# Kernel optimization log

Hardware: AMD Instinct MI355X
Metric: run time of the kernel (lower is better)

Reference implementation:

```python
import jax, jax.numpy as jnp
import numpy as np
import math

NUM_HEADS = 4
PH, PW = 8, 8

def setup_inputs() -> dict:
    key = jax.random.key(0)
    ks = jax.random.split(key, 12)
    B, C, H, W = 2, 128, 256, 256
    x = jax.random.normal(ks[0], (B, C, H, W), dtype=jnp.float32)
    mask = jax.random.uniform(ks[1], (B, 1, H, W), dtype=jnp.float32)
    s1 = 1.0 / math.sqrt(C)          # kaiming-ish scale for 1x1 convs
    s3 = 1.0 / math.sqrt(C * 9)      # 3x3 conv
    wq = jax.random.normal(ks[2], (C, C), dtype=jnp.float32) * s1
    bq = jax.random.normal(ks[3], (C,), dtype=jnp.float32) * 0.01
    wk = jax.random.normal(ks[4], (C, C), dtype=jnp.float32) * s1
    bk = jax.random.normal(ks[5], (C,), dtype=jnp.float32) * 0.01
    wv = jax.random.normal(ks[6], (C, C), dtype=jnp.float32) * s1
    bv = jax.random.normal(ks[7], (C,), dtype=jnp.float32) * 0.01
    wo = jax.random.normal(ks[8], (C, C, 3, 3), dtype=jnp.float32) * s3
    bo = jax.random.normal(ks[9], (C,), dtype=jnp.float32) * 0.01
    return {"x": x, "mask": mask, "wq": wq, "bq": bq, "wk": wk, "bk": bk,
            "wv": wv, "bv": bv, "wo": wo, "bo": bo}

def _conv1x1(x, w, b):
    # w: [O, I]; x: [B, C, H, W]
    return jnp.einsum('oc,bchw->bohw', w, x) + b[None, :, None, None]

def _window(t, b, heads, dph, out_h, out_w):
    # [B, C, H, W] -> [B, heads, out_h*out_w, dph*PH*PW]
    t = t.reshape(b, heads, dph, out_h, PH, out_w, PW)
    t = t.transpose(0, 1, 3, 5, 2, 4, 6)
    return t.reshape(b, heads, out_h * out_w, dph * PH * PW)

def reference(x, mask, wq, bq, wk, bk, wv, bv, wo, bo):
    b, c, h, w = x.shape
    heads = NUM_HEADS
    dph = c // heads
    out_h, out_w = h // PH, w // PW
    d = dph * PH * PW

    q = _window(_conv1x1(x, wq, bq), b, heads, dph, out_h, out_w)
    k = _window(_conv1x1(x, wk, bk), b, heads, dph, out_h, out_w)
    v = _window(_conv1x1(x, wv, bv), b, heads, dph, out_h, out_w)

    # NOTE: original torch code calls att.masked_fill(mask, -1e9) without
    # assignment (not in-place), so the mask has no effect on the output.
    att = jnp.einsum('bhqd,bhkd->bhqk', q, k) * (1.0 / math.sqrt(d))
    p = jax.nn.softmax(att, axis=-1)
    y = jnp.einsum('bhqk,bhkd->bhqd', p, v)

    # un-window: [B, heads, S, d] -> [B, C, H, W]
    y = y.reshape(b, heads, out_h, out_w, dph, PH, PW)
    y = y.transpose(0, 1, 4, 2, 5, 3, 6).reshape(b, c, h, w)

    # output: reflect-padded 3x3 conv + LeakyReLU(0.2)
    yp = jnp.pad(y, ((0, 0), (0, 0), (1, 1), (1, 1)), mode='reflect')
    out = jax.lax.conv_general_dilated(
        yp, wo, window_strides=(1, 1), padding='VALID',
        dimension_numbers=('NCHW', 'OIHW', 'NCHW')) + bo[None, :, None, None]
    return jnp.where(out > 0, out, 0.2 * out)
```

## Files before the change

kernel.cpp:

```cpp
#include <hip/hip_runtime.h>
#include <hip/hip_bf16.h>
#include <stdint.h>

typedef unsigned short u16;
typedef __attribute__((ext_vector_type(8))) short bf16x8;
typedef __attribute__((ext_vector_type(4))) short bf16x4;
typedef __attribute__((ext_vector_type(4))) float f32x4;
typedef __attribute__((ext_vector_type(4))) unsigned short u16x4;

__device__ __forceinline__ float bf2f(u16 u) {
  union { unsigned i; float f; } c; c.i = ((unsigned)u) << 16; return c.f;
}
__device__ __forceinline__ u16 f2bf(float f) {
  union { float f; unsigned i; } c; c.f = f;
  unsigned r = c.i + 0x7FFFu + ((c.i >> 16) & 1u);
  return (u16)(r >> 16);
}
__device__ __forceinline__ unsigned cvt_pk(float lo, float hi) {
  unsigned r;
  asm("v_cvt_pk_bf16_f32 %0, %1, %2" : "=v"(r) : "v"(lo), "v"(hi));
  return r;
}
__device__ __forceinline__ void gl2lds16(const u16* g, u16* l) {
  __builtin_amdgcn_global_load_lds(
      (const __attribute__((address_space(1))) unsigned int*)(uintptr_t)g,
      (__attribute__((address_space(3))) unsigned int*)(uintptr_t)l,
      16, 0, 0);
}

__global__ void k_prep(const float* __restrict__ wo, const float* __restrict__ wq,
                       const float* __restrict__ wk, const float* __restrict__ wv,
                       u16* __restrict__ WT, u16* __restrict__ WQKV) {
  int i = blockIdx.x * 256 + threadIdx.x;
  if (i < 9 * 128 * 128) {
    int c = i & 127;
    int o = (i >> 7) & 127;
    int tap = i >> 14;
    WT[i] = f2bf(wo[((o * 128 + c) * 3 + tap / 3) * 3 + tap % 3]);
  } else {
    int j = i - 9 * 128 * 128;
    if (j < 3 * 16384) {
      int sel = j >> 14, rest = j & 16383;
      const float* w = sel == 0 ? wq : (sel == 1 ? wk : wv);
      WQKV[j] = f2bf(w[rest]);
    }
  }
}

__global__ __launch_bounds__(256) void k_qkv(
    const float* __restrict__ x, const u16* __restrict__ WQKV,
    const float* __restrict__ bq, const float* __restrict__ bk,
    const float* __restrict__ bv,
    u16* __restrict__ Q, u16* __restrict__ K, u16* __restrict__ V) {
  const int blk = blockIdx.x;
  const int b = blk >> 9;
  const int t = blk & 511;
  const int th = t & 31, tw = t >> 5;
  const int h0 = th * 8, w0 = tw * 16;
  const int s0 = th * 32 + tw * 2;
  const int tid = threadIdx.x, lane = tid & 63, wid = tid >> 6;
  const int wr = wid >> 1, wc = wid & 1;
  const int g = lane >> 4, l15 = lane & 15;

  __shared__ u16 Ot[128 * 136];

  bf16x8 bfrag[4][4];
  {
    const float* xb = x + (size_t)b * 8388608 + (size_t)(g * 8) * 65536
                        + (h0 + wc * 4) * 256 + w0 + l15;
    #pragma unroll
    for (int ks = 0; ks < 4; ++ks)
      #pragma unroll
      for (int e2 = 0; e2 < 4; ++e2) {
        const float* pa = xb + (size_t)(ks * 32 + e2 * 2) * 65536;
        const float* pb = pa + 65536;
        #pragma unroll
        for (int n = 0; n < 4; ++n)
          ((unsigned*)&bfrag[ks][n])[e2] = cvt_pk(pa[n * 256], pb[n * 256]);
      }
  }

  for (int sel = 0; sel < 3; ++sel) {
    const u16* w = WQKV + sel * 16384;
    const float* bias = sel == 0 ? bq : (sel == 1 ? bk : bv);
    u16* qkv = sel == 0 ? Q : (sel == 1 ? K : V);

    f32x4 acc[4][4] = {};
    #pragma unroll
    for (int ks = 0; ks < 4; ++ks) {
      bf16x8 a[4];
      #pragma unroll
      for (int m = 0; m < 4; ++m) {
        int o = wr * 64 + m * 16 + l15;
        a[m] = *(const bf16x8*)(w + o * 128 + ks * 32 + g * 8);
      }
      #pragma unroll
      for (int m = 0; m < 4; ++m)
        #pragma unroll
        for (int n = 0; n < 4; ++n)
          acc[m][n] = __builtin_amdgcn_mfma_f32_16x16x32_bf16(a[m], bfrag[ks][n], acc[m][n], 0, 0, 0);
    }

    float4 bias4[4];
    #pragma unroll
    for (int m = 0; m < 4; ++m)
      bias4[m] = *(const float4*)&bias[wr * 64 + m * 16 + g * 4];

    __syncthreads();
    #pragma unroll
    for (int m = 0; m < 4; ++m) {
      int o0 = wr * 64 + m * 16 + g * 4;
      #pragma unroll
      for (int n = 0; n < 4; ++n) {
        int p = wc * 64 + n * 16 + l15;
        unsigned r0 = cvt_pk(acc[m][n][0] + bias4[m].x, acc[m][n][1] + bias4[m].y);
        unsigned r1 = cvt_pk(acc[m][n][2] + bias4[m].z, acc[m][n][3] + bias4[m].w);
        unsigned* dp = (unsigned*)&Ot[p * 136 + o0];
        dp[0] = r0; dp[1] = r1;
      }
    }
    __syncthreads();
    #pragma unroll
    for (int it = 0; it < 8; ++it) {
      int head = it >> 1, s2 = it & 1;
      int pixw = tid >> 2;
      int dphc = tid & 3;
      int pl = (pixw >> 3) * 16 + s2 * 8 + (pixw & 7);
      bf16x8 vv = *(const bf16x8*)&Ot[pl * 136 + head * 32 + dphc * 8];
      size_t gaddr = ((size_t)((b * 4 + head) * 1024 + s0 + s2)) * 2048 + pixw * 32 + dphc * 8;
      *(bf16x8*)(qkv + gaddr) = vv;
    }
  }
}

__global__ __launch_bounds__(256) void k_qkvt(const u16* __restrict__ Q,
                                              const u16* __restrict__ K,
                                              u16* __restrict__ ATT,
                                              const u16* __restrict__ V,
                                              u16* __restrict__ VT) {
  __shared__ __align__(16) u16 smem[17408];
  const int tid = threadIdx.x, lane = tid & 63, wid = tid >> 6;

  if (blockIdx.x < 512) {
    const int bh = blockIdx.x & 7;
    const int tile = blockIdx.x >> 3;
    const int tm = tile & 7, tn = tile >> 3;
    const int row0 = tm * 128, col0 = tn * 128;
    const int wr = wid >> 1, wc = wid & 1;
    const u16* Ab = Q + (size_t)bh * 1024 * 2048 + (size_t)row0 * 2048;
    const u16* Bb = K + (size_t)bh * 1024 * 2048 + (size_t)col0 * 2048;
    f32x4 acc[4][4] = {};
    const int lr = lane >> 2, lc = lane & 3;
    const int scs = lc ^ ((lr >> 1) & 3);
    const int rsw = ((lane & 15) >> 1) & 3;

    auto stage = [&](int k0, int bf) {
      u16* As = smem + bf * 8192;
      u16* Bs = smem + 4096 + bf * 8192;
      const u16* s0 = Ab + (size_t)(wid * 16 + lr) * 2048 + k0 + scs * 8;
      gl2lds16(s0, &As[wid * 512]);
      gl2lds16(s0 + (size_t)64 * 2048, &As[2048 + wid * 512]);
      const u16* s1 = Bb + (size_t)(wid * 16 + lr) * 2048 + k0 + scs * 8;
      gl2lds16(s1, &Bs[wid * 512]);
      gl2lds16(s1 + (size_t)64 * 2048, &Bs[2048 + wid * 512]);
    };

    stage(0, 0);
    asm volatile("s_waitcnt vmcnt(0)" ::: "memory");
    __syncthreads();
    int cur = 0;
    for (int k0 = 0; k0 < 2048; k0 += 32) {
      if (k0 + 32 < 2048) stage(k0 + 32, cur ^ 1);
      const u16* As = smem + cur * 8192;
      const u16* Bs = smem + 4096 + cur * 8192;
      bf16x8 a[4], bb[4];
      const int g = lane >> 4;
      const int chp = (g ^ rsw) * 8;
      #pragma unroll
      for (int m = 0; m < 4; ++m)
        a[m] = *(const bf16x8*)&As[(wr * 64 + m * 16 + (lane & 15)) * 32 + chp];
      #pragma unroll
      for (int n = 0; n < 4; ++n)
        bb[n] = *(const bf16x8*)&Bs[(wc * 64 + n * 16 + (lane & 15)) * 32 + chp];
      #pragma unroll
      for (int m = 0; m < 4; ++m)
        #pragma unroll
        for (int n = 0; n < 4; ++n)
          acc[m][n] = __builtin_amdgcn_mfma_f32_16x16x32_bf16(a[m], bb[n], acc[m][n], 0, 0, 0);
      asm volatile("s_waitcnt vmcnt(0)" ::: "memory");
      __syncthreads();
      cur ^= 1;
    }
    const float scale = 0.02209708691207961f;
    u16* Ot = smem;
    #pragma unroll
    for (int m = 0; m < 4; ++m) {
      int r0 = wr * 64 + m * 16 + ((lane >> 4) << 2);
      #pragma unroll
      for (int n = 0; n < 4; ++n) {
        int dv = wc * 64 + n * 16 + (lane & 15);
        #pragma unroll
        for (int j = 0; j < 4; ++j)
          Ot[(r0 + j) * 136 + dv] = f2bf(acc[m][n][j] * scale);
      }
    }
    __syncthreads();
    u16* outb = ATT + (size_t)bh * 1024 * 1024 + (size_t)row0 * 1024 + col0;
    #pragma unroll
    for (int it = 0; it < 8; ++it) {
      int ci = it * 256 + tid;
      int sl = ci >> 4;
      int ch = ci & 15;
      bf16x8 vv = *(const bf16x8*)&Ot[sl * 136 + ch * 8];
      *(bf16x8*)(outb + (size_t)sl * 1024 + ch * 8) = vv;
    }
  } else {
    const int idx = blockIdx.x - 512;
    const int bh = idx & 7;
    const int t2 = idx >> 3;
    const int ts = t2 & 7, td = t2 >> 3;
    const int s0 = ts * 128, d0 = td * 128;
    u16* T = smem;
    const u16* Vb = V + (size_t)bh * 1024 * 2048 + (size_t)s0 * 2048 + d0;

    #pragma unroll
    for (int pass = 0; pass < 8; ++pass) {
      int r = pass * 16 + (tid >> 4);
      int c8 = (tid & 15) * 8;
      union { uint4 u; u16 e[8]; } d;
      d.u = *(const uint4*)(Vb + (size_t)r * 2048 + c8);
      int chunk = (r >> 3) ^ ((c8 >> 3) & 15);
      #pragma unroll
      for (int e = 0; e < 8; ++e)
        T[(c8 + e) * 128 + chunk * 8 + (r & 7)] = d.e[e];
    }
    __syncthreads();
    u16* VTb = VT + (size_t)bh * 2048 * 1024 + (size_t)d0 * 1024 + s0;
    #pragma unroll
    for (int pass = 0; pass < 8; ++pass) {
      int rd = pass * 16 + (tid >> 4);
      int c8 = (tid & 15) * 8;
      int chunk = (c8 >> 3) ^ ((rd >> 3) & 15);
      bf16x8 v = *(const bf16x8*)&T[rd * 128 + chunk * 8];
      *(bf16x8*)(VTb + (size_t)rd * 1024 + c8) = v;
    }
  }
}

__global__ __launch_bounds__(256) void k_softmax(const u16* __restrict__ ATT,
                                                 u16* __restrict__ P) {
  const int row = blockIdx.x;
  const u16* a = ATT + (size_t)row * 1024;
  const int tid = threadIdx.x;
  u16x4 raw = *(const u16x4*)(a + tid * 4);
  float v0 = bf2f(raw[0]), v1 = bf2f(raw[1]), v2 = bf2f(raw[2]), v3 = bf2f(raw[3]);
  float mx = fmaxf(fmaxf(v0, v1), fmaxf(v2, v3));
  #pragma unroll
  for (int off = 32; off; off >>= 1) mx = fmaxf(mx, __shfl_xor(mx, off, 64));
  __shared__ float red[8];
  if ((tid & 63) == 0) red[tid >> 6] = mx;
  __syncthreads();
  mx = fmaxf(fmaxf(red[0], red[1]), fmaxf(red[2], red[3]));
  float e0 = __expf(v0 - mx), e1 = __expf(v1 - mx);
  float e2 = __expf(v2 - mx), e3 = __expf(v3 - mx);
  float s = e0 + e1 + e2 + e3;
  #pragma unroll
  for (int off = 32; off; off >>= 1) s += __shfl_xor(s, off, 64);
  if ((tid & 63) == 0) red[4 + (tid >> 6)] = s;
  __syncthreads();
  s = red[4] + red[5] + red[6] + red[7];
  float inv = 1.0f / s;
  u16x4 o = { f2bf(e0 * inv), f2bf(e1 * inv), f2bf(e2 * inv), f2bf(e3 * inv) };
  *(u16x4*)(P + (size_t)row * 1024 + tid * 4) = o;
}

__global__ __launch_bounds__(256) void k_pv(const u16* __restrict__ P,
                                            const u16* __restrict__ VT,
                                            u16* __restrict__ Yn) {
  const int bh = blockIdx.x & 7;
  const int tile = blockIdx.x >> 3;
  const int tm = tile & 7, tn = tile >> 3;
  const int row0 = tm * 128, col0 = tn * 128;
  const int tid = threadIdx.x, lane = tid & 63, wid = tid >> 6;
  const int wr = wid >> 1, wc = wid & 1;
  __shared__ __align__(16) u16 smem[17408];
  u16* Ot = smem;
  const u16* Pb = P + (size_t)bh * 1024 * 1024 + (size_t)row0 * 1024;
  const u16* VTb = VT + (size_t)bh * 2048 * 1024 + (size_t)col0 * 1024;
  f32x4 acc[4][4] = {};
  const int lr = lane >> 2, lc = lane & 3;
  const int scs = lc ^ ((lr >> 1) & 3);
  const int rsw = ((lane & 15) >> 1) & 3;

  auto stage = [&](int k0, int bf) {
    u16* As = smem + bf * 8192;
    u16* Bs = smem + 4096 + bf * 8192;
    const u16* s0 = Pb + (size_t)(wid * 16 + lr) * 1024 + k0 + scs * 8;
    gl2lds16(s0, &As[wid * 512]);
    gl2lds16(s0 + (size_t)64 * 1024, &As[2048 + wid * 512]);
    const u16* s1 = VTb + (size_t)(wid * 16 + lr) * 1024 + k0 + scs * 8;
    gl2lds16(s1, &Bs[wid * 512]);
    gl2lds16(s1 + (size_t)64 * 1024, &Bs[2048 + wid * 512]);
  };

  stage(0, 0);
  asm volatile("s_waitcnt vmcnt(0)" ::: "memory");
  __syncthreads();
  int cur = 0;
  for (int k0 = 0; k0 < 1024; k0 += 32) {
    if (k0 + 32 < 1024) stage(k0 + 32, cur ^ 1);
    const u16* As = smem + cur * 8192;
    const u16* Bs = smem + 4096 + cur * 8192;
    bf16x8 a[4], bb[4];
    const int g = lane >> 4;
    const int chp = (g ^ rsw) * 8;
    #pragma unroll
    for (int m = 0; m < 4; ++m)
      a[m] = *(const bf16x8*)&As[(wr * 64 + m * 16 + (lane & 15)) * 32 + chp];
    #pragma unroll
    for (int n = 0; n < 4; ++n)
      bb[n] = *(const bf16x8*)&Bs[(wc * 64 + n * 16 + (lane & 15)) * 32 + chp];
    #pragma unroll
    for (int m = 0; m < 4; ++m)
      #pragma unroll
      for (int n = 0; n < 4; ++n)
        acc[m][n] = __builtin_amdgcn_mfma_f32_16x16x32_bf16(a[m], bb[n], acc[m][n], 0, 0, 0);
    asm volatile("s_waitcnt vmcnt(0)" ::: "memory");
    __syncthreads();
    cur ^= 1;
  }

  #pragma unroll
  for (int m = 0; m < 4; ++m) {
    int r0 = wr * 64 + m * 16 + ((lane >> 4) << 2);
    #pragma unroll
    for (int n = 0; n < 4; ++n) {
      int dv = wc * 64 + n * 16 + (lane & 15);
      #pragma unroll
      for (int j = 0; j < 4; ++j)
        Ot[(r0 + j) * 136 + dv] = f2bf(acc[m][n][j]);
    }
  }
  __syncthreads();
  const int b = bh >> 2, head = bh & 3;
  const int pixw0 = tn * 4;
  #pragma unroll
  for (int it = 0; it < 8; ++it) {
    int ci = it * 256 + tid;
    int sl = ci >> 4;
    int pxl = (ci >> 2) & 3;
    int dc = ci & 3;
    bf16x8 vv = *(const bf16x8*)&Ot[sl * 136 + pxl * 32 + dc * 8];
    int s = row0 + sl, oh = s >> 5, ow = s & 31;
    int pixw = pixw0 + pxl, ph = pixw >> 3, pw = pixw & 7;
    int h = oh * 8 + ph, w2 = ow * 8 + pw;
    size_t gaddr = (((size_t)(b * 256 + h) * 256) + w2) * 128 + head * 32 + dc * 8;
    *(bf16x8*)(Yn + gaddr) = vv;
  }
}

__global__ __launch_bounds__(512, 2) void k_conv(const u16* __restrict__ Yn,
                                                 const u16* __restrict__ WT,
                                                 const float* __restrict__ bo,
                                                 float* __restrict__ out) {
  const int wgid = blockIdx.x;
  const int r7 = wgid & 7;
  const int b = (r7 >> 2) & 1;
  const int w0 = ((r7 >> 1) & 1) * 128;
  const int h0 = ((r7 & 1) * 32 + (wgid >> 3)) * 4;
  const int tid = threadIdx.x, lane = tid & 63, wid = tid >> 6;
  const int wo_ = wid & 1;
  const int wh = wid >> 1;
  const int g = lane >> 4, l15 = lane & 15;
  __shared__ u16 S[6][136 * 64];
  __shared__ u16 WTl[2][8192];
  f32x4 acc[4][8] = {};

  auto stageS = [&](int chalf) {
    for (int g5 = wid; g5 < 102; g5 += 8) {
      int rowi = g5 / 17, grp = g5 % 17;
      int rg = grp * 8 + (lane >> 3);
      int chunk = lane & 7;
      int row = h0 + rowi - 1;
      row = row < 0 ? 1 : (row > 255 ? 254 : row);
      int wsrc = w0 - 1 + rg;
      wsrc = wsrc < 0 ? 1 : (wsrc > 255 ? 254 : wsrc);
      const u16* src = Yn + ((size_t)(b * 256 + row) * 256 + wsrc) * 128 + chalf * 64
                         + ((chunk ^ (rg & 7)) * 8);
      gl2lds16(src, &S[rowi][grp * 512]);
    }
  };
  auto stageWT = [&](int chalf, int tap, int nb) {
    #pragma unroll
    for (int r2 = 0; r2 < 2; ++r2) {
      int g5 = wid + r2 * 8;
      int orow = g5 * 8 + (lane >> 3);
      int csrc = (lane & 7) ^ (lane >> 3);
      const u16* src = WT + ((size_t)tap * 128 + orow) * 128 + chalf * 64 + csrc * 8;
      gl2lds16(src, &WTl[nb][g5 * 512]);
    }
  };

  int buf = 0;
  stageS(0);
  stageWT(0, 0, 0);
  asm volatile("s_waitcnt vmcnt(0)" ::: "memory");
  __syncthreads();

  #pragma unroll
  for (int chalf = 0; chalf < 2; ++chalf) {
    if (chalf) {
      __syncthreads();
      stageS(1);
      stageWT(1, 0, buf ^ 1);
      asm volatile("s_waitcnt vmcnt(0)" ::: "memory");
      __syncthreads();
      buf ^= 1;
    }
    #pragma unroll
    for (int ky = 0; ky < 3; ++ky) {
      #pragma unroll
      for (int kx = 0; kx < 3; ++kx) {
        const int tap = ky * 3 + kx;
        const bool hasNext = (tap < 8);
        if (hasNext) stageWT(chalf, tap + 1, buf ^ 1);
        bf16x8 areg[2][4];
        #pragma unroll
        for (int ckh = 0; ckh < 2; ++ckh)
          #pragma unroll
          for (int m = 0; m < 4; ++m) {
            int o = wo_ * 64 + m * 16 + l15;
            int cc2 = ((ckh << 2) + g) ^ (o & 7);
            areg[ckh][m] = *(const bf16x8*)&WTl[buf][o * 64 + cc2 * 8];
          }
        #pragma unroll
        for (int ckh = 0; ckh < 2; ++ckh) {
          #pragma unroll
          for (int nh = 0; nh < 2; ++nh) {
            bf16x8 bb[4];
            #pragma unroll
            for (int n4 = 0; n4 < 4; ++n4) {
              int p = (nh * 4 + n4) * 16 + l15 + kx;
              int chunk = ((ckh << 2) + g) ^ (p & 7);
              bb[n4] = *(const bf16x8*)&S[wh + ky][p * 64 + chunk * 8];
            }
            #pragma unroll
            for (int m = 0; m < 4; ++m)
              #pragma unroll
              for (int n4 = 0; n4 < 4; ++n4)
                acc[m][nh * 4 + n4] = __builtin_amdgcn_mfma_f32_16x16x32_bf16(
                    areg[ckh][m], bb[n4], acc[m][nh * 4 + n4], 0, 0, 0);
          }
        }
        if (hasNext) {
          asm volatile("s_waitcnt vmcnt(0)" ::: "memory");
          __syncthreads();
          buf ^= 1;
        }
      }
    }
  }
  #pragma unroll
  for (int m = 0; m < 4; ++m) {
    int o0 = wo_ * 64 + m * 16 + (g << 2);
    #pragma unroll
    for (int n = 0; n < 8; ++n) {
      int p = n * 16 + l15;
      #pragma unroll
      for (int j = 0; j < 4; ++j) {
        int o = o0 + j;
        float v = acc[m][n][j] + bo[o];
        v = v > 0.f ? v : 0.2f * v;
        out[(((size_t)b * 128 + o) << 16) + ((h0 + wh) << 8) + w0 + p] = v;
      }
    }
  }
}

extern "C" void kernel_launch(void* const* d_in, const int* in_sizes, int n_in,
                              void* d_out, int out_size, void* d_ws, size_t ws_size,
                              hipStream_t stream) {
  const float* x  = (const float*)d_in[0];
  const float* wq = (const float*)d_in[2];
  const float* bq = (const float*)d_in[3];
  const float* wk = (const float*)d_in[4];
  const float* bk = (const float*)d_in[5];
  const float* wv = (const float*)d_in[6];
  const float* bv = (const float*)d_in[7];
  const float* wo = (const float*)d_in[8];
  const float* bo = (const float*)d_in[9];

  char* ws = (char*)d_ws;
  u16*   WT   = (u16*)(ws);
  u16*   WQKV = (u16*)(ws + (size_t)(512 << 10));
  u16*   Q   = (u16*)(ws + (size_t)(1  << 20));
  u16*   K   = (u16*)(ws + (size_t)(33 << 20));
  u16*   V   = (u16*)(ws + (size_t)(65 << 20));
  u16*   ATT = (u16*)(ws + (size_t)(97 << 20));
  u16*   P   = (u16*)(ws + (size_t)(129 << 20));
  u16*   Yn  = (u16*)(ws + (size_t)(145 << 20));
  u16*   VT  = (u16*)(ws + (size_t)(177 << 20));
  float* outp = (float*)d_out;

  k_prep<<<768, 256, 0, stream>>>(wo, wq, wk, wv, WT, WQKV);
  k_qkv<<<1024, 256, 0, stream>>>(x, WQKV, bq, bk, bv, Q, K, V);
  k_qkvt<<<1536, 256, 0, stream>>>(Q, K, ATT, V, VT);
  k_softmax<<<8192, 256, 0, stream>>>(ATT, P);
  k_pv<<<1024, 256, 0, stream>>>(P, VT, Yn);
  k_conv<<<256, 512, 0, stream>>>(Yn, WT, bo, outp);
}
```

Before: 209.9 us.

## Fuse softmax into QK^T and PV epilogues with atomic row sums

Removes the standalone softmax kernel. The QK^T epilogue now writes exp(score) directly and accumulates per-row sums into a float buffer with atomics; that buffer is zeroed in the prep kernel. The PV epilogue then divides its output by the row sum. This avoids one full read and write of the attention matrix and a kernel launch. The cost is dropping the max subtraction, so exp can overflow if scores grow large, plus atomic traffic and float-order nondeterminism in the sums.

```diff
diff --git a/kernel.cpp b/kernel.cpp
--- a/kernel.cpp
+++ b/kernel.cpp
@@ -30,20 +30,22 @@
 
 __global__ void k_prep(const float* __restrict__ wo, const float* __restrict__ wq,
                        const float* __restrict__ wk, const float* __restrict__ wv,
-                       u16* __restrict__ WT, u16* __restrict__ WQKV) {
+                       u16* __restrict__ WT, u16* __restrict__ WQKV,
+                       float* __restrict__ RS) {
   int i = blockIdx.x * 256 + threadIdx.x;
   if (i < 9 * 128 * 128) {
     int c = i & 127;
     int o = (i >> 7) & 127;
     int tap = i >> 14;
     WT[i] = f2bf(wo[((o * 128 + c) * 3 + tap / 3) * 3 + tap % 3]);
+  } else if (i < 9 * 128 * 128 + 3 * 16384) {
+    int j = i - 9 * 128 * 128;
+    int sel = j >> 14, rest = j & 16383;
+    const float* w = sel == 0 ? wq : (sel == 1 ? wk : wv);
+    WQKV[j] = f2bf(w[rest]);
   } else {
-    int j = i - 9 * 128 * 128;
-    if (j < 3 * 16384) {
-      int sel = j >> 14, rest = j & 16383;
-      const float* w = sel == 0 ? wq : (sel == 1 ? wk : wv);
-      WQKV[j] = f2bf(w[rest]);
-    }
+    int rsi = i - (9 * 128 * 128 + 3 * 16384);
+    if (rsi < 8192) RS[rsi] = 0.f;
   }
 }
 
@@ -135,9 +137,10 @@
 
 __global__ __launch_bounds__(256) void k_qkvt(const u16* __restrict__ Q,
                                               const u16* __restrict__ K,
-                                              u16* __restrict__ ATT,
+                                              u16* __restrict__ EATT,
                                               const u16* __restrict__ V,
-                                              u16* __restrict__ VT) {
+                                              u16* __restrict__ VT,
+                                              float* __restrict__ RS) {
   __shared__ __align__(16) u16 smem[17408];
   const int tid = threadIdx.x, lane = tid & 63, wid = tid >> 6;
 
@@ -193,19 +196,39 @@
     }
     const float scale = 0.02209708691207961f;
     u16* Ot = smem;
+    float psum[4][4];
     #pragma unroll
     for (int m = 0; m < 4; ++m) {
       int r0 = wr * 64 + m * 16 + ((lane >> 4) << 2);
+      #pragma unroll
+      for (int j = 0; j < 4; ++j) psum[m][j] = 0.f;
       #pragma unroll
       for (int n = 0; n < 4; ++n) {
         int dv = wc * 64 + n * 16 + (lane & 15);
         #pragma unroll
-        for (int j = 0; j < 4; ++j)
-          Ot[(r0 + j) * 136 + dv] = f2bf(acc[m][n][j] * scale);
-      }
-    }
+        for (int j = 0; j < 4; ++j) {
+          float e = __expf(acc[m][n][j] * scale);
+          Ot[(r0 + j) * 136 + dv] = f2bf(e);
+          psum[m][j] += e;
+        }
+      }
+    }
+    #pragma unroll
+    for (int m = 0; m < 4; ++m)
+      #pragma unroll
+      for (int j = 0; j < 4; ++j) {
+        float v = psum[m][j];
+        v += __shfl_xor(v, 1, 64);
+        v += __shfl_xor(v, 2, 64);
+        v += __shfl_xor(v, 4, 64);
+        v += __shfl_xor(v, 8, 64);
+        if ((lane & 15) == 0) {
+          int r = row0 + wr * 64 + m * 16 + ((lane >> 4) << 2) + j;
+          atomicAdd(&RS[bh * 1024 + r], v);
+        }
+      }
     __syncthreads();
-    u16* outb = ATT + (size_t)bh * 1024 * 1024 + (size_t)row0 * 1024 + col0;
+    u16* outb = EATT + (size_t)bh * 1024 * 1024 + (size_t)row0 * 1024 + col0;
     #pragma unroll
     for (int it = 0; it < 8; ++it) {
       int ci = it * 256 + tid;
@@ -247,35 +270,9 @@
   }
 }
 
-__global__ __launch_bounds__(256) void k_softmax(const u16* __restrict__ ATT,
-                                                 u16* __restrict__ P) {
-  const int row = blockIdx.x;
-  const u16* a = ATT + (size_t)row * 1024;
-  const int tid = threadIdx.x;
-  u16x4 raw = *(const u16x4*)(a + tid * 4);
-  float v0 = bf2f(raw[0]), v1 = bf2f(raw[1]), v2 = bf2f(raw[2]), v3 = bf2f(raw[3]);
-  float mx = fmaxf(fmaxf(v0, v1), fmaxf(v2, v3));
-  #pragma unroll
-  for (int off = 32; off; off >>= 1) mx = fmaxf(mx, __shfl_xor(mx, off, 64));
-  __shared__ float red[8];
-  if ((tid & 63) == 0) red[tid >> 6] = mx;
-  __syncthreads();
-  mx = fmaxf(fmaxf(red[0], red[1]), fmaxf(red[2], red[3]));
-  float e0 = __expf(v0 - mx), e1 = __expf(v1 - mx);
-  float e2 = __expf(v2 - mx), e3 = __expf(v3 - mx);
-  float s = e0 + e1 + e2 + e3;
-  #pragma unroll
-  for (int off = 32; off; off >>= 1) s += __shfl_xor(s, off, 64);
-  if ((tid & 63) == 0) red[4 + (tid >> 6)] = s;
-  __syncthreads();
-  s = red[4] + red[5] + red[6] + red[7];
-  float inv = 1.0f / s;
-  u16x4 o = { f2bf(e0 * inv), f2bf(e1 * inv), f2bf(e2 * inv), f2bf(e3 * inv) };
-  *(u16x4*)(P + (size_t)row * 1024 + tid * 4) = o;
-}
-
-__global__ __launch_bounds__(256) void k_pv(const u16* __restrict__ P,
+__global__ __launch_bounds__(256) void k_pv(const u16* __restrict__ EATT,
                                             const u16* __restrict__ VT,
+                                            const float* __restrict__ RS,
                                             u16* __restrict__ Yn) {
   const int bh = blockIdx.x & 7;
   const int tile = blockIdx.x >> 3;
@@ -285,7 +282,7 @@
   const int wr = wid >> 1, wc = wid & 1;
   __shared__ __align__(16) u16 smem[17408];
   u16* Ot = smem;
-  const u16* Pb = P + (size_t)bh * 1024 * 1024 + (size_t)row0 * 1024;
+  const u16* Pb = EATT + (size_t)bh * 1024 * 1024 + (size_t)row0 * 1024;
   const u16* VTb = VT + (size_t)bh * 2048 * 1024 + (size_t)col0 * 1024;
   f32x4 acc[4][4] = {};
   const int lr = lane >> 2, lc = lane & 3;
@@ -333,12 +330,16 @@
   #pragma unroll
   for (int m = 0; m < 4; ++m) {
     int r0 = wr * 64 + m * 16 + ((lane >> 4) << 2);
+    float inv[4];
+    #pragma unroll
+    for (int j = 0; j < 4; ++j)
+      inv[j] = 1.0f / RS[bh * 1024 + row0 + r0 + j];
     #pragma unroll
     for (int n = 0; n < 4; ++n) {
       int dv = wc * 64 + n * 16 + (lane & 15);
       #pragma unroll
       for (int j = 0; j < 4; ++j)
-        Ot[(r0 + j) * 136 + dv] = f2bf(acc[m][n][j]);
+        Ot[(r0 + j) * 136 + dv] = f2bf(acc[m][n][j] * inv[j]);
     }
   }
   __syncthreads();
@@ -496,16 +497,15 @@
   u16*   Q   = (u16*)(ws + (size_t)(1  << 20));
   u16*   K   = (u16*)(ws + (size_t)(33 << 20));
   u16*   V   = (u16*)(ws + (size_t)(65 << 20));
-  u16*   ATT = (u16*)(ws + (size_t)(97 << 20));
-  u16*   P   = (u16*)(ws + (size_t)(129 << 20));
+  u16*   EATT= (u16*)(ws + (size_t)(97 << 20));
+  float* RS  = (float*)(ws + (size_t)(129 << 20));
   u16*   Yn  = (u16*)(ws + (size_t)(145 << 20));
   u16*   VT  = (u16*)(ws + (size_t)(177 << 20));
   float* outp = (float*)d_out;
 
-  k_prep<<<768, 256, 0, stream>>>(wo, wq, wk, wv, WT, WQKV);
+  k_prep<<<800, 256, 0, stream>>>(wo, wq, wk, wv, WT, WQKV, RS);
   k_qkv<<<1024, 256, 0, stream>>>(x, WQKV, bq, bk, bv, Q, K, V);
-  k_qkvt<<<1536, 256, 0, stream>>>(Q, K, ATT, V, VT);
-  k_softmax<<<8192, 256, 0, stream>>>(ATT, P);
-  k_pv<<<1024, 256, 0, stream>>>(P, VT, Yn);
+  k_qkvt<<<1536, 256, 0, stream>>>(Q, K, EATT, V, VT, RS);
+  k_pv<<<1024, 256, 0, stream>>>(EATT, VT, RS, Yn);
   k_conv<<<256, 512, 0, stream>>>(Yn, WT, bo, outp);
 }
```

Result: faster. 201.1 us (-4.2%).
